# Optimization experiments

Hardware: AMD Instinct MI355X
Metric: run time of the kernel (lower is better)

Reference implementation:

```python
import jax, jax.numpy as jnp
import numpy as np

MASK_ID = -100
L, D, HID, NH = 10, 768, 3072, 12
DH = D // NH
REACH = 2  # (sliding_window_size - 1) // 2 with window 5


def _layernorm(x, g, b, eps=1e-5):
    mu = x.mean(-1, keepdims=True)
    var = ((x - mu) ** 2).mean(-1, keepdims=True)
    return (x - mu) * jax.lax.rsqrt(var + eps) * g + b


def _adaln(x, temb, w, bb, g, be):
    # AdaLayerNormShiftScale: linear(silu(temb)) -> (scale, shift)
    e = jax.nn.silu(temb) @ w + bb
    scale, shift = jnp.split(e, 2, axis=-1)
    return _layernorm(x, g, be) * (1.0 + scale) + shift


def _timestep_emb(t):
    half = D // 2
    exponent = -np.log(10000.0) * jnp.arange(half, dtype=jnp.float32) / (half - 1.0)
    freq = jnp.exp(exponent)  # [half]
    emb = t.astype(jnp.float32)[..., None] * freq  # [b,s,half]
    return jnp.concatenate([jnp.sin(emb), jnp.cos(emb)], axis=-1)  # [b,s,D]


def setup_inputs():
    key = jax.random.key(0)
    ks = jax.random.split(key, 16)
    b, s = 4, 1024
    # packed token ids: 4 samples of 256 tokens (16x16 grid), last 64 tokens padding
    idx = np.arange(s)
    sid = idx // 256
    hpos = (idx % 256) // 16
    wpos = idx % 16
    sid = np.where(idx >= 960, MASK_ID, sid)
    tok = np.stack([sid, hpos, wpos], axis=-1)  # [s,3]
    token_ids = jnp.asarray(np.broadcast_to(tok, (b, s, 3)).copy(), dtype=jnp.int32)
    t = jax.random.randint(ks[0], (b, 1), 0, L + 1).astype(jnp.int32)
    t = jnp.broadcast_to(t, (b, s))

    def w(k, shape):
        return jax.random.normal(k, shape, jnp.float32) * 0.02

    return dict(
        x=jax.random.normal(ks[1], (b, s, D), jnp.float32),
        t=t,
        token_ids=token_ids,
        proj_in_w=w(ks[2], (D, D)), proj_in_b=jnp.zeros((D,), jnp.float32),
        h_emb=w(ks[3], (64, D)), w_emb=w(ks[4], (64, D)),
        adaln1_w=w(ks[5], (L, D, 2 * D)), adaln1_b=jnp.zeros((L, 2 * D), jnp.float32),
        ln1_g=jnp.ones((L, D), jnp.float32), ln1_b=jnp.zeros((L, D), jnp.float32),
        qkv_w=w(ks[6], (L, D, 3 * D)), qkv_b=jnp.zeros((L, 3 * D), jnp.float32),
        o_w=w(ks[7], (L, D, D)), o_b=jnp.zeros((L, D), jnp.float32),
        adaln2_w=w(ks[8], (L, D, 2 * D)), adaln2_b=jnp.zeros((L, 2 * D), jnp.float32),
        ln2_g=jnp.ones((L, D), jnp.float32), ln2_b=jnp.zeros((L, D), jnp.float32),
        fc1_w=w(ks[9], (L, D, HID)), fc1_b=jnp.zeros((L, HID), jnp.float32),
        fc2_w=w(ks[10], (L, HID, D)), fc2_b=jnp.zeros((L, D), jnp.float32),
        nout_w=w(ks[11], (D, 2 * D)), nout_b=jnp.zeros((2 * D,), jnp.float32),
        nout_g=jnp.ones((D,), jnp.float32), nout_beta=jnp.zeros((D,), jnp.float32),
    )


def _encoder(x, t, token_ids, proj_in_w, proj_in_b, h_emb, w_emb,
             adaln1_w, adaln1_b, ln1_g, ln1_b, qkv_w, qkv_b, o_w, o_b,
             adaln2_w, adaln2_b, ln2_g, ln2_b, fc1_w, fc1_b, fc2_w, fc2_b,
             nout_w, nout_b, nout_g, nout_beta):
    b, s, _ = x.shape
    sample_ids = token_ids[..., 0]          # [b,s]
    pos = token_ids[..., 1:]                # [b,s,2]
    x = x @ proj_in_w + proj_in_b
    x = x + h_emb[pos[..., 0]] + w_emb[pos[..., 1]]

    # block-sparse mask: same packed sample, Chebyshev sliding window, no padding queries
    same = sample_ids[:, :, None] == sample_ids[:, None, :]              # [b,s,s]
    cheby = jnp.abs(pos[:, :, None, :] - pos[:, None, :, :]).max(-1)      # [b,s,s]
    notpad_q = (sample_ids != MASK_ID)[:, :, None]
    mask = same & (cheby <= REACH) & notpad_q                             # [b,s,s]
    row_valid = mask.any(-1)[..., None]                                   # [b,s,1]

    temb = _timestep_emb(t)  # [b,s,D]
    scale = 1.0 / np.sqrt(DH)
    for i in range(L):
        h1 = _adaln(x, temb, adaln1_w[i], adaln1_b[i], ln1_g[i], ln1_b[i])
        qkv = h1 @ qkv_w[i] + qkv_b[i]
        q, k, v = jnp.split(qkv, 3, axis=-1)
        q = q.reshape(b, s, NH, DH)
        k = k.reshape(b, s, NH, DH)
        v = v.reshape(b, s, NH, DH)
        scores = jnp.einsum('bqhd,bkhd->bhqk', q, k) * scale
        scores = jnp.where(mask[:, None], scores, -1e30)
        attn = jax.nn.softmax(scores, axis=-1)
        o = jnp.einsum('bhqk,bkhd->bqhd', attn, v).reshape(b, s, D)
        o = jnp.where(row_valid, o, 0.0)  # fully-masked (padding) rows -> 0
        x = x + o @ o_w[i] + o_b[i]
        h2 = _adaln(x, temb, adaln2_w[i], adaln2_b[i], ln2_g[i], ln2_b[i])
        x = x + jax.nn.gelu(h2 @ fc1_w[i] + fc1_b[i], approximate=False) @ fc2_w[i] + fc2_b[i]
    x = _adaln(x, temb, nout_w, nout_b, nout_g, nout_beta)
    return x


def reference(x, t, token_ids, proj_in_w, proj_in_b, h_emb, w_emb,
              adaln1_w, adaln1_b, ln1_g, ln1_b, qkv_w, qkv_b, o_w, o_b,
              adaln2_w, adaln2_b, ln2_g, ln2_b, fc1_w, fc1_b, fc2_w, fc2_b,
              nout_w, nout_b, nout_g, nout_beta):
    return _encoder(x, t, token_ids, proj_in_w, proj_in_b, h_emb, w_emb,
                    adaln1_w, adaln1_b, ln1_g, ln1_b, qkv_w, qkv_b, o_w, o_b,
                    adaln2_w, adaln2_b, ln2_g, ln2_b, fc1_w, fc1_b, fc2_w, fc2_b,
                    nout_w, nout_b, nout_g, nout_beta)
```

## Files before the change

### kernel.cpp

```cpp
#include <hip/hip_runtime.h>
#include <hip/hip_bf16.h>
#include <math.h>

#define MASK_ID (-100)
#define SEQ 1024
#define BATCH 4
#define DMODEL 768
#define NHEAD 12
#define DHEAD 64
#define NLAYER 10
#define HIDDEN 3072

typedef unsigned short ushort_t;
typedef unsigned int uint_t;

__device__ __forceinline__ ushort_t f2bf(float f) {
    uint_t u = __float_as_uint(f);
    u = u + 0x7fffu + ((u >> 16) & 1u);
    return (ushort_t)(u >> 16);
}
__device__ __forceinline__ float bf2f(ushort_t u) {
    return __uint_as_float(((uint_t)u) << 16);
}

__device__ __forceinline__ void async_ld16(ushort_t* lds, const ushort_t* g) {
    __builtin_amdgcn_global_load_lds((__attribute__((address_space(1))) const void*)g,
                                     (__attribute__((address_space(3))) void*)lds, 16, 0, 0);
}

#define WAITVM(n) asm volatile("s_waitcnt vmcnt(" #n ")" ::: "memory")

__global__ void temb_silu_kernel(const int* __restrict__ t, float* __restrict__ stemb) {
    int b = blockIdx.x;
    int j = threadIdx.x;
    float tv = (float)t[b * SEQ];
    float freq = expf(-logf(10000.f) * (float)j / 383.f);
    float arg = tv * freq;
    float s = sinf(arg), c = cosf(arg);
    stemb[b * DMODEL + j]       = s / (1.f + expf(-s));
    stemb[b * DMODEL + 384 + j] = c / (1.f + expf(-c));
}

__global__ __launch_bounds__(256)
void adaln_partial_kernel(const float* __restrict__ stemb,
                          const float* __restrict__ a1w,
                          const float* __restrict__ a2w,
                          const float* __restrict__ nw,
                          float* __restrict__ partial) {
    int chunk = blockIdx.x;
    int kc    = blockIdx.y;
    int slot  = blockIdx.z;
    int tid = threadIdx.x;
    int col = chunk * 256 + tid;
    const float* W;
    if (slot == 20) W = nw;
    else {
        int i = slot >> 1;
        W = ((slot & 1) ? a2w : a1w) + (size_t)i * DMODEL * 2 * DMODEL;
    }
    __shared__ float sb[4 * 96];
    for (int idx = tid; idx < 4 * 96; idx += 256) {
        int bb = idx / 96, kk = idx % 96;
        sb[idx] = stemb[bb * DMODEL + kc * 96 + kk];
    }
    __syncthreads();
    const float* Wp = W + (size_t)(kc * 96) * (2 * DMODEL) + col;
    float a0 = 0.f, a1 = 0.f, a2 = 0.f, a3 = 0.f;
    #pragma unroll 4
    for (int kk = 0; kk < 96; ++kk) {
        float w = Wp[(size_t)kk * (2 * DMODEL)];
        a0 = fmaf(sb[kk], w, a0);
        a1 = fmaf(sb[96 + kk], w, a1);
        a2 = fmaf(sb[192 + kk], w, a2);
        a3 = fmaf(sb[288 + kk], w, a3);
    }
    size_t base = ((size_t)(slot * 8 + kc) * 4) * (2 * DMODEL) + col;
    partial[base + 0 * 2 * DMODEL] = a0;
    partial[base + 1 * 2 * DMODEL] = a1;
    partial[base + 2 * 2 * DMODEL] = a2;
    partial[base + 3 * 2 * DMODEL] = a3;
}

__global__ __launch_bounds__(256)
void adaln_reduce_kernel(const float* __restrict__ partial,
                         const float* __restrict__ a1b, const float* __restrict__ a2b,
                         const float* __restrict__ nb,
                         float* __restrict__ e_all) {
    int chunk = blockIdx.x;
    int slot  = blockIdx.y;
    int col = chunk * 256 + threadIdx.x;
    const float* bb;
    if (slot == 20) bb = nb;
    else {
        int i = slot >> 1;
        bb = ((slot & 1) ? a2b : a1b) + i * 2 * DMODEL;
    }
    float bias = bb[col];
    float s0 = bias, s1 = bias, s2 = bias, s3 = bias;
    #pragma unroll
    for (int kc = 0; kc < 8; ++kc) {
        size_t base = ((size_t)(slot * 8 + kc) * 4) * (2 * DMODEL) + col;
        s0 += partial[base + 0 * 2 * DMODEL];
        s1 += partial[base + 1 * 2 * DMODEL];
        s2 += partial[base + 2 * 2 * DMODEL];
        s3 += partial[base + 3 * 2 * DMODEL];
    }
    size_t o = (size_t)slot * 4 * (2 * DMODEL) + col;
    e_all[o + 0 * 2 * DMODEL] = s0;
    e_all[o + 1 * 2 * DMODEL] = s1;
    e_all[o + 2 * 2 * DMODEL] = s2;
    e_all[o + 3 * 2 * DMODEL] = s3;
}

__global__ __launch_bounds__(256)
void transpose_bf16_kernel(const float* __restrict__ in, ushort_t* __restrict__ out,
                           int R, int C) {
    __shared__ float tile[32][33];
    int tx = threadIdx.x & 31, ty = threadIdx.x >> 5;
    int c0 = blockIdx.x * 32, r0 = blockIdx.y * 32;
    #pragma unroll
    for (int i = 0; i < 4; ++i)
        tile[ty + 8 * i][tx] = in[(size_t)(r0 + ty + 8 * i) * C + c0 + tx];
    __syncthreads();
    #pragma unroll
    for (int i = 0; i < 4; ++i)
        out[(size_t)(c0 + ty + 8 * i) * R + r0 + tx] = f2bf(tile[tx][ty + 8 * i]);
}

__global__ __launch_bounds__(256)
void transpose_all_kernel(const float* __restrict__ w0, const float* __restrict__ w1,
                          const float* __restrict__ w2, const float* __restrict__ w3,
                          ushort_t* __restrict__ o0, ushort_t* __restrict__ o1,
                          ushort_t* __restrict__ o2, ushort_t* __restrict__ o3) {
    int layer = blockIdx.y;
    int id = blockIdx.x;
    const float* in; ushort_t* out; int R, C, tile_id, TX;
    if (id < 216) {
        in = w0 + (size_t)layer * DMODEL * 3 * DMODEL; out = o0 + (size_t)layer * 3 * DMODEL * DMODEL;
        R = DMODEL; C = 3 * DMODEL; tile_id = id; TX = 36;
    } else if (id < 288) {
        in = w1 + (size_t)layer * DMODEL * DMODEL; out = o1 + (size_t)layer * DMODEL * DMODEL;
        R = DMODEL; C = DMODEL; tile_id = id - 216; TX = 12;
    } else if (id < 576) {
        in = w2 + (size_t)layer * DMODEL * HIDDEN; out = o2 + (size_t)layer * HIDDEN * DMODEL;
        R = DMODEL; C = HIDDEN; tile_id = id - 288; TX = 48;
    } else {
        in = w3 + (size_t)layer * HIDDEN * DMODEL; out = o3 + (size_t)layer * DMODEL * HIDDEN;
        R = HIDDEN; C = DMODEL; tile_id = id - 576; TX = 12;
    }
    int c0 = (tile_id % TX) * 64, r0 = (tile_id / TX) * 128;
    __shared__ float tl[128][65];
    int tid = threadIdx.x;
    #pragma unroll
    for (int i = 0; i < 32; ++i) {
        int idx = i * 256 + tid;
        int r = idx >> 6, c = idx & 63;
        tl[r][c] = in[(size_t)(r0 + r) * C + c0 + c];
    }
    __syncthreads();
    #pragma unroll
    for (int j = 0; j < 16; ++j) {
        int idx = j * 256 + tid;
        int oc = idx >> 6, pr = idx & 63;
        float a = tl[pr * 2][oc], b = tl[pr * 2 + 1][oc];
        uint_t pk = (uint_t)f2bf(a) | ((uint_t)f2bf(b) << 16);
        *(uint_t*)&out[(size_t)(c0 + oc) * R + r0 + pr * 2] = pk;
    }
}

__global__ __launch_bounds__(256)
void f32_to_bf16_kernel(const float* __restrict__ in, ushort_t* __restrict__ out, int n8) {
    int i = blockIdx.x * 256 + threadIdx.x;
    if (i >= n8) return;
    float4 a = ((const float4*)in)[2 * i];
    float4 b = ((const float4*)in)[2 * i + 1];
    uint4 o;
    o.x = (uint_t)f2bf(a.x) | ((uint_t)f2bf(a.y) << 16);
    o.y = (uint_t)f2bf(a.z) | ((uint_t)f2bf(a.w) << 16);
    o.z = (uint_t)f2bf(b.x) | ((uint_t)f2bf(b.y) << 16);
    o.w = (uint_t)f2bf(b.z) | ((uint_t)f2bf(b.w) << 16);
    ((uint4*)out)[i] = o;
}

template<int OUT_BF>
__global__ __launch_bounds__(256)
void ln_adaln_kernel(const float* __restrict__ in, void* __restrict__ outv,
                     const float* __restrict__ g, const float* __restrict__ be,
                     const float* __restrict__ e) {
    int wid = threadIdx.x >> 6, lane = threadIdx.x & 63;
    int row = blockIdx.x * 4 + wid;
    int b = row >> 10;
    const float* xr = in + (size_t)row * DMODEL;
    float v[12];
    float s = 0.f, ss = 0.f;
    #pragma unroll
    for (int j = 0; j < 12; ++j) {
        v[j] = xr[lane + j * 64];
        s += v[j];
        ss = fmaf(v[j], v[j], ss);
    }
    #pragma unroll
    for (int o = 1; o < 64; o <<= 1) { s += __shfl_xor(s, o); ss += __shfl_xor(ss, o); }
    float mu = s * (1.f / DMODEL);
    float var = ss * (1.f / DMODEL) - mu * mu;
    float rs = rsqrtf(var + 1e-5f);
    const float* esc = e + (size_t)b * (2 * DMODEL);
    #pragma unroll
    for (int j = 0; j < 12; ++j) {
        int c = lane + j * 64;
        float y = (v[j] - mu) * rs * g[c] + be[c];
        y = y * (1.f + esc[c]) + esc[DMODEL + c];
        if (OUT_BF) ((ushort_t*)outv)[(size_t)row * DMODEL + c] = f2bf(y);
        else        ((float*)outv)[(size_t)row * DMODEL + c] = y;
    }
}

__device__ __forceinline__ float gelu_exact(float x) {
    return 0.5f * x * (1.f + erff(x * 0.70710678118654752f));
}

template<int BM, int BN, int EPI, int OCC>
__global__ __launch_bounds__(256, OCC)
void gemm_bf16(const ushort_t* __restrict__ A, const ushort_t* __restrict__ Wt,
               const float* __restrict__ bias, void* __restrict__ outv,
               const float* __restrict__ emb_h, const float* __restrict__ emb_w,
               const int* __restrict__ tok,
               int M, int N, int K) {
    constexpr int WM = BM / 2, WN = BN / 2;
    constexpr int FM = WM / 16, FN = WN / 16;
    constexpr int BUF = (BM + BN) * 64;
    constexpr int LPT = (BM + BN) / 32;
    using f32x4  = __attribute__((ext_vector_type(4))) float;
    using bf16x8 = __attribute__((ext_vector_type(8))) short;

    __shared__ __align__(16) ushort_t lds[3 * BUF];

    int tid = threadIdx.x;
    int lane = tid & 63, wid = tid >> 6;
    int wr = wid >> 1, wc = wid & 1;
    int l16 = lane & 15, lg = lane >> 4;
    int sw = l16 & 7;

    int nx = N / BN;
    int cpx = gridDim.x >> 3;
    int wg = blockIdx.x;
    int wgid = (wg & 7) * cpx + (wg >> 3);
    int bx = wgid % nx, by = wgid / nx;
    int bm0 = by * BM, bn0 = bx * BN;

    f32x4 acc[FM][FN];
    #pragma unroll
    for (int m = 0; m < FM; ++m)
        #pragma unroll
        for (int n = 0; n < FN; ++n)
            #pragma unroll
            for (int r = 0; r < 4; ++r) acc[m][n][r] = 0.f;

    const ushort_t* Abase = A + (size_t)bm0 * K;
    const ushort_t* Bbase = Wt + (size_t)bn0 * K;

    #define STAGE(bufi, kt)                                                             \
        do {                                                                            \
            _Pragma("unroll")                                                           \
            for (int s2 = 0; s2 < BM / 32; ++s2) {                                      \
                int ca = s2 * 256 + tid;                                                \
                int rw = ca >> 3, kcs = (ca & 7) ^ (rw & 7);                            \
                async_ld16(&lds[(bufi) * BUF + ca * 8],                                 \
                           Abase + (size_t)rw * K + (kt) * 64 + kcs * 8);               \
            }                                                                           \
            _Pragma("unroll")                                                           \
            for (int s2 = 0; s2 < BN / 32; ++s2) {                                      \
                int ca = s2 * 256 + tid;                                                \
                int rw = ca >> 3, kcs = (ca & 7) ^ (rw & 7);                            \
                async_ld16(&lds[(bufi) * BUF + BM * 64 + ca * 8],                       \
                           Bbase + (size_t)rw * K + (kt) * 64 + kcs * 8);               \
            }                                                                           \
        } while (0)

    int nk = K >> 6;
    STAGE(0, 0);
    STAGE(1, 1);
    int bufi = 0;
    for (int kt = 0; kt < nk; ++kt) {
        int nxt = bufi + 2; if (nxt >= 3) nxt -= 3;
        if (kt + 2 < nk) {
            STAGE(nxt, kt + 2);
            if constexpr (LPT == 4) WAITVM(8); else WAITVM(12);
        } else if (kt + 1 < nk) {
            if constexpr (LPT == 4) WAITVM(4); else WAITVM(6);
        } else {
            WAITVM(0);
        }
        __builtin_amdgcn_s_barrier();
        __builtin_amdgcn_s_setprio(1);
        #pragma unroll
        for (int kk = 0; kk < 2; ++kk) {
            bf16x8 af[FM], bfr[FN];
            #pragma unroll
            for (int m = 0; m < FM; ++m) {
                int row = wr * WM + m * 16 + l16;
                int csw = (kk * 4 + lg) ^ sw;
                af[m] = *(const bf16x8*)&lds[bufi * BUF + row * 64 + csw * 8];
            }
            #pragma unroll
            for (int n = 0; n < FN; ++n) {
                int row = wc * WN + n * 16 + l16;
                int csw = (kk * 4 + lg) ^ sw;
                bfr[n] = *(const bf16x8*)&lds[bufi * BUF + BM * 64 + row * 64 + csw * 8];
            }
            #pragma unroll
            for (int m = 0; m < FM; ++m)
                #pragma unroll
                for (int n = 0; n < FN; ++n)
                    acc[m][n] = __builtin_amdgcn_mfma_f32_16x16x32_bf16(af[m], bfr[n], acc[m][n], 0, 0, 0);
        }
        __builtin_amdgcn_s_setprio(0);
        __builtin_amdgcn_s_barrier();
        ++bufi; if (bufi >= 3) bufi = 0;
    }
    #undef STAGE

    int r0 = bm0 + wr * WM, c0 = bn0 + wc * WN;
    #pragma unroll
    for (int m = 0; m < FM; ++m) {
        #pragma unroll
        for (int n = 0; n < FN; ++n) {
            int cc = c0 + n * 16 + l16;
            float bcol = bias[cc];
            #pragma unroll
            for (int r = 0; r < 4; ++r) {
                int row = r0 + m * 16 + lg * 4 + r;
                float v = acc[m][n][r] + bcol;
                if (EPI == 0) {
                    ((ushort_t*)outv)[(size_t)row * N + cc] = f2bf(v);
                } else if (EPI == 1) {
                    int p0 = tok[row * 3 + 1], p1 = tok[row * 3 + 2];
                    v += emb_h[p0 * DMODEL + cc] + emb_w[p1 * DMODEL + cc];
                    ((float*)outv)[(size_t)row * N + cc] = v;
                } else if (EPI == 2) {
                    float* op = (float*)outv + (size_t)row * N + cc;
                    *op = *op + v;
                } else {
                    ((ushort_t*)outv)[(size_t)row * N + cc] = f2bf(gelu_exact(v));
                }
            }
        }
    }
}

__global__ __launch_bounds__(256)
void attn_kernel(const ushort_t* __restrict__ qkv, const int* __restrict__ tok,
                 ushort_t* __restrict__ o_out) {
    int tid = threadIdx.x;
    int u = tid >> 2, part = tid & 3;
    int q = blockIdx.x * 16 + (u & 15);
    int h = blockIdx.y * 4 + (u >> 4);
    int b = blockIdx.z;
    int m = b * SEQ + q;
    ushort_t* op = o_out + (size_t)m * DMODEL + h * DHEAD + part * 16;
    int sid = tok[m * 3];
    if (sid == MASK_ID) {
        uint4 z = {0u, 0u, 0u, 0u};
        ((uint4*)op)[0] = z;
        ((uint4*)op)[1] = z;
        return;
    }
    int qh = tok[m * 3 + 1], qw = tok[m * 3 + 2];
    const ushort_t* qp = qkv + (size_t)m * (3 * DMODEL) + h * DHEAD + part * 16;
    float qv[16], ov[16];
    {
        uint4 u0 = ((const uint4*)qp)[0];
        uint4 u1 = ((const uint4*)qp)[1];
        qv[0] = bf2f(u0.x & 0xffff); qv[1] = bf2f(u0.x >> 16);
        qv[2] = bf2f(u0.y & 0xffff); qv[3] = bf2f(u0.y >> 16);
        qv[4] = bf2f(u0.z & 0xffff); qv[5] = bf2f(u0.z >> 16);
        qv[6] = bf2f(u0.w & 0xffff); qv[7] = bf2f(u0.w >> 16);
        qv[8]  = bf2f(u1.x & 0xffff); qv[9]  = bf2f(u1.x >> 16);
        qv[10] = bf2f(u1.y & 0xffff); qv[11] = bf2f(u1.y >> 16);
        qv[12] = bf2f(u1.z & 0xffff); qv[13] = bf2f(u1.z >> 16);
        qv[14] = bf2f(u1.w & 0xffff); qv[15] = bf2f(u1.w >> 16);
    }
    #pragma unroll
    for (int i = 0; i < 16; ++i) ov[i] = 0.f;
    float mx = -1e30f, den = 0.f;
    for (int dh = -2; dh <= 2; ++dh) {
        for (int dw = -2; dw <= 2; ++dw) {
            int kq = q + dh * 16 + dw;
            if (kq < 0 || kq >= SEQ) continue;
            int km = b * SEQ + kq;
            if (tok[km * 3] != sid) continue;
            int kh2 = tok[km * 3 + 1], kw2 = tok[km * 3 + 2];
            int adh = kh2 - qh; if (adh < 0) adh = -adh;
            int adw = kw2 - qw; if (adw < 0) adw = -adw;
            if (adh > 2 || adw > 2) continue;
            const ushort_t* kp = qkv + (size_t)km * (3 * DMODEL) + DMODEL + h * DHEAD + part * 16;
            float dot;
            {
                uint4 u0 = ((const uint4*)kp)[0];
                uint4 u1 = ((const uint4*)kp)[1];
                dot = qv[0] * bf2f(u0.x & 0xffff);
                dot = fmaf(qv[1], bf2f(u0.x >> 16), dot);
                dot = fmaf(qv[2], bf2f(u0.y & 0xffff), dot);
                dot = fmaf(qv[3], bf2f(u0.y >> 16), dot);
                dot = fmaf(qv[4], bf2f(u0.z & 0xffff), dot);
                dot = fmaf(qv[5], bf2f(u0.z >> 16), dot);
                dot = fmaf(qv[6], bf2f(u0.w & 0xffff), dot);
                dot = fmaf(qv[7], bf2f(u0.w >> 16), dot);
                dot = fmaf(qv[8],  bf2f(u1.x & 0xffff), dot);
                dot = fmaf(qv[9],  bf2f(u1.x >> 16), dot);
                dot = fmaf(qv[10], bf2f(u1.y & 0xffff), dot);
                dot = fmaf(qv[11], bf2f(u1.y >> 16), dot);
                dot = fmaf(qv[12], bf2f(u1.z & 0xffff), dot);
                dot = fmaf(qv[13], bf2f(u1.z >> 16), dot);
                dot = fmaf(qv[14], bf2f(u1.w & 0xffff), dot);
                dot = fmaf(qv[15], bf2f(u1.w >> 16), dot);
            }
            dot += __shfl_xor(dot, 1);
            dot += __shfl_xor(dot, 2);
            float sc = dot * 0.125f;
            float nm = fmaxf(mx, sc);
            float c1 = expf(mx - nm);
            float c2 = expf(sc - nm);
            den = den * c1 + c2;
            const ushort_t* vp = qkv + (size_t)km * (3 * DMODEL) + 2 * DMODEL + h * DHEAD + part * 16;
            {
                uint4 u0 = ((const uint4*)vp)[0];
                uint4 u1 = ((const uint4*)vp)[1];
                ov[0] = ov[0] * c1 + c2 * bf2f(u0.x & 0xffff);
                ov[1] = ov[1] * c1 + c2 * bf2f(u0.x >> 16);
                ov[2] = ov[2] * c1 + c2 * bf2f(u0.y & 0xffff);
                ov[3] = ov[3] * c1 + c2 * bf2f(u0.y >> 16);
                ov[4] = ov[4] * c1 + c2 * bf2f(u0.z & 0xffff);
                ov[5] = ov[5] * c1 + c2 * bf2f(u0.z >> 16);
                ov[6] = ov[6] * c1 + c2 * bf2f(u0.w & 0xffff);
                ov[7] = ov[7] * c1 + c2 * bf2f(u0.w >> 16);
                ov[8]  = ov[8]  * c1 + c2 * bf2f(u1.x & 0xffff);
                ov[9]  = ov[9]  * c1 + c2 * bf2f(u1.x >> 16);
                ov[10] = ov[10] * c1 + c2 * bf2f(u1.y & 0xffff);
                ov[11] = ov[11] * c1 + c2 * bf2f(u1.y >> 16);
                ov[12] = ov[12] * c1 + c2 * bf2f(u1.z & 0xffff);
                ov[13] = ov[13] * c1 + c2 * bf2f(u1.z >> 16);
                ov[14] = ov[14] * c1 + c2 * bf2f(u1.w & 0xffff);
                ov[15] = ov[15] * c1 + c2 * bf2f(u1.w >> 16);
            }
            mx = nm;
        }
    }
    float inv = 1.f / den;
    uint4 o0, o1;
    o0.x = (uint_t)f2bf(ov[0] * inv) | ((uint_t)f2bf(ov[1] * inv) << 16);
    o0.y = (uint_t)f2bf(ov[2] * inv) | ((uint_t)f2bf(ov[3] * inv) << 16);
    o0.z = (uint_t)f2bf(ov[4] * inv) | ((uint_t)f2bf(ov[5] * inv) << 16);
    o0.w = (uint_t)f2bf(ov[6] * inv) | ((uint_t)f2bf(ov[7] * inv) << 16);
    o1.x = (uint_t)f2bf(ov[8]  * inv) | ((uint_t)f2bf(ov[9]  * inv) << 16);
    o1.y = (uint_t)f2bf(ov[10] * inv) | ((uint_t)f2bf(ov[11] * inv) << 16);
    o1.z = (uint_t)f2bf(ov[12] * inv) | ((uint_t)f2bf(ov[13] * inv) << 16);
    o1.w = (uint_t)f2bf(ov[14] * inv) | ((uint_t)f2bf(ov[15] * inv) << 16);
    ((uint4*)op)[0] = o0;
    ((uint4*)op)[1] = o1;
}

extern "C" void kernel_launch(void* const* d_in, const int* in_sizes, int n_in,
                              void* d_out, int out_size, void* d_ws, size_t ws_size,
                              hipStream_t stream) {
    const float* x_in      = (const float*)d_in[0];
    const int*   t         = (const int*)d_in[1];
    const int*   tok       = (const int*)d_in[2];
    const float* proj_in_w = (const float*)d_in[3];
    const float* proj_in_b = (const float*)d_in[4];
    const float* h_emb     = (const float*)d_in[5];
    const float* w_emb     = (const float*)d_in[6];
    const float* adaln1_w  = (const float*)d_in[7];
    const float* adaln1_b  = (const float*)d_in[8];
    const float* ln1_g     = (const float*)d_in[9];
    const float* ln1_b     = (const float*)d_in[10];
    const float* qkv_w     = (const float*)d_in[11];
    const float* qkv_b     = (const float*)d_in[12];
    const float* o_w       = (const float*)d_in[13];
    const float* o_b       = (const float*)d_in[14];
    const float* adaln2_w  = (const float*)d_in[15];
    const float* adaln2_b  = (const float*)d_in[16];
    const float* ln2_g     = (const float*)d_in[17];
    const float* ln2_b     = (const float*)d_in[18];
    const float* fc1_w     = (const float*)d_in[19];
    const float* fc1_b     = (const float*)d_in[20];
    const float* fc2_w     = (const float*)d_in[21];
    const float* fc2_b     = (const float*)d_in[22];
    const float* nout_w    = (const float*)d_in[23];
    const float* nout_b    = (const float*)d_in[24];
    const float* nout_g    = (const float*)d_in[25];
    const float* nout_beta = (const float*)d_in[26];

    const int M = BATCH * SEQ;

    float* stemb   = (float*)d_ws;
    float* e_all   = stemb + BATCH * DMODEL;
    float* partial = e_all + 21 * BATCH * 2 * DMODEL;
    ushort_t* h_bf   = (ushort_t*)(partial + 21 * 8 * 4 * 2 * DMODEL);
    ushort_t* qkv_bf = h_bf + (size_t)M * DMODEL;
    ushort_t* hid_bf = qkv_bf + (size_t)M * 3 * DMODEL;
    ushort_t* projT  = hid_bf + (size_t)M * HIDDEN;
    ushort_t* qkvT_a = projT + (size_t)DMODEL * DMODEL;
    ushort_t* oT_a   = qkvT_a + (size_t)NLAYER * 3 * DMODEL * DMODEL;
    ushort_t* fc1T_a = oT_a + (size_t)NLAYER * DMODEL * DMODEL;
    ushort_t* fc2T_a = fc1T_a + (size_t)NLAYER * DMODEL * HIDDEN;
    float* x = (float*)d_out;

    temb_silu_kernel<<<BATCH, 384, 0, stream>>>(t, stemb);
    adaln_partial_kernel<<<dim3(6, 8, 2 * NLAYER + 1), 256, 0, stream>>>(
        stemb, adaln1_w, adaln2_w, nout_w, partial);
    adaln_reduce_kernel<<<dim3(6, 2 * NLAYER + 1), 256, 0, stream>>>(
        partial, adaln1_b, adaln2_b, nout_b, e_all);

    transpose_all_kernel<<<dim3(864, NLAYER), 256, 0, stream>>>(
        qkv_w, o_w, fc1_w, fc2_w, qkvT_a, oT_a, fc1T_a, fc2T_a);
    transpose_bf16_kernel<<<dim3(DMODEL / 32, DMODEL / 32), 256, 0, stream>>>(proj_in_w, projT, DMODEL, DMODEL);

    f32_to_bf16_kernel<<<(M * DMODEL / 8 + 255) / 256, 256, 0, stream>>>(x_in, h_bf, M * DMODEL / 8);
    gemm_bf16<64, 64, 1, 3><<<(DMODEL / 64) * (M / 64), 256, 0, stream>>>(
        h_bf, projT, proj_in_b, x, h_emb, w_emb, tok, M, DMODEL, DMODEL);

    for (int i = 0; i < NLAYER; ++i) {
        ln_adaln_kernel<1><<<M / 4, 256, 0, stream>>>(
            x, h_bf, ln1_g + i * DMODEL, ln1_b + i * DMODEL,
            e_all + (size_t)(2 * i) * BATCH * 2 * DMODEL);
        gemm_bf16<64, 128, 0, 2><<<(3 * DMODEL / 128) * (M / 64), 256, 0, stream>>>(
            h_bf, qkvT_a + (size_t)i * 3 * DMODEL * DMODEL, qkv_b + i * 3 * DMODEL,
            qkv_bf, nullptr, nullptr, nullptr, M, 3 * DMODEL, DMODEL);
        attn_kernel<<<dim3(SEQ / 16, NHEAD / 4, BATCH), 256, 0, stream>>>(qkv_bf, tok, h_bf);
        gemm_bf16<64, 64, 2, 3><<<(DMODEL / 64) * (M / 64), 256, 0, stream>>>(
            h_bf, oT_a + (size_t)i * DMODEL * DMODEL, o_b + i * DMODEL,
            x, nullptr, nullptr, nullptr, M, DMODEL, DMODEL);
        ln_adaln_kernel<1><<<M / 4, 256, 0, stream>>>(
            x, h_bf, ln2_g + i * DMODEL, ln2_b + i * DMODEL,
            e_all + (size_t)(2 * i + 1) * BATCH * 2 * DMODEL);
        gemm_bf16<64, 128, 3, 2><<<(HIDDEN / 128) * (M / 64), 256, 0, stream>>>(
            h_bf, fc1T_a + (size_t)i * DMODEL * HIDDEN, fc1_b + i * HIDDEN,
            hid_bf, nullptr, nullptr, nullptr, M, HIDDEN, DMODEL);
        gemm_bf16<64, 64, 2, 3><<<(DMODEL / 64) * (M / 64), 256, 0, stream>>>(
            hid_bf, fc2T_a + (size_t)i * DMODEL * HIDDEN, fc2_b + i * DMODEL,
            x, nullptr, nullptr, nullptr, M, DMODEL, HIDDEN);
    }

    ln_adaln_kernel<0><<<M / 4, 256, 0, stream>>>(
        x, x, nout_g, nout_beta, e_all + (size_t)(2 * NLAYER) * BATCH * 2 * DMODEL);
}
```

Before: 1.839 ms.

## Use 128x128 single-buffer GEMM for QKV/FC1 and shrink transpose tiles

Adds a new gemm_bf16_big kernel with 128x128 block tiles, 4x4 MFMA fragments per wave, XCD-aware block remapping and a single LDS buffer, and uses it for the QKV and FC1 projections. The larger tile raises arithmetic intensity per loaded byte, but the single buffer gives up the triple-buffered load/compute overlap of the old kernel. The weight transpose kernel also switches to 64x64 tiles staged in LDS as bf16, halving shared memory and doubling the grid.

```diff
diff --git a/kernel.cpp b/kernel.cpp
--- a/kernel.cpp
+++ b/kernel.cpp
@@ -135,35 +135,34 @@
     int layer = blockIdx.y;
     int id = blockIdx.x;
     const float* in; ushort_t* out; int R, C, tile_id, TX;
-    if (id < 216) {
+    if (id < 432) {
         in = w0 + (size_t)layer * DMODEL * 3 * DMODEL; out = o0 + (size_t)layer * 3 * DMODEL * DMODEL;
         R = DMODEL; C = 3 * DMODEL; tile_id = id; TX = 36;
-    } else if (id < 288) {
+    } else if (id < 576) {
         in = w1 + (size_t)layer * DMODEL * DMODEL; out = o1 + (size_t)layer * DMODEL * DMODEL;
-        R = DMODEL; C = DMODEL; tile_id = id - 216; TX = 12;
-    } else if (id < 576) {
+        R = DMODEL; C = DMODEL; tile_id = id - 432; TX = 12;
+    } else if (id < 1152) {
         in = w2 + (size_t)layer * DMODEL * HIDDEN; out = o2 + (size_t)layer * HIDDEN * DMODEL;
-        R = DMODEL; C = HIDDEN; tile_id = id - 288; TX = 48;
+        R = DMODEL; C = HIDDEN; tile_id = id - 576; TX = 48;
     } else {
         in = w3 + (size_t)layer * HIDDEN * DMODEL; out = o3 + (size_t)layer * DMODEL * HIDDEN;
-        R = HIDDEN; C = DMODEL; tile_id = id - 576; TX = 12;
-    }
-    int c0 = (tile_id % TX) * 64, r0 = (tile_id / TX) * 128;
-    __shared__ float tl[128][65];
+        R = HIDDEN; C = DMODEL; tile_id = id - 1152; TX = 12;
+    }
+    int c0 = (tile_id % TX) * 64, r0 = (tile_id / TX) * 64;
+    __shared__ ushort_t tlb[64 * 65];
     int tid = threadIdx.x;
     #pragma unroll
-    for (int i = 0; i < 32; ++i) {
+    for (int i = 0; i < 16; ++i) {
         int idx = i * 256 + tid;
         int r = idx >> 6, c = idx & 63;
-        tl[r][c] = in[(size_t)(r0 + r) * C + c0 + c];
+        tlb[r * 65 + c] = f2bf(in[(size_t)(r0 + r) * C + c0 + c]);
     }
     __syncthreads();
     #pragma unroll
-    for (int j = 0; j < 16; ++j) {
+    for (int j = 0; j < 8; ++j) {
         int idx = j * 256 + tid;
-        int oc = idx >> 6, pr = idx & 63;
-        float a = tl[pr * 2][oc], b = tl[pr * 2 + 1][oc];
-        uint_t pk = (uint_t)f2bf(a) | ((uint_t)f2bf(b) << 16);
+        int oc = idx >> 5, pr = idx & 31;
+        uint_t pk = (uint_t)tlb[(pr * 2) * 65 + oc] | ((uint_t)tlb[(pr * 2 + 1) * 65 + oc] << 16);
         *(uint_t*)&out[(size_t)(c0 + oc) * R + r0 + pr * 2] = pk;
     }
 }
@@ -217,6 +216,94 @@
 
 __device__ __forceinline__ float gelu_exact(float x) {
     return 0.5f * x * (1.f + erff(x * 0.70710678118654752f));
+}
+
+template<int EPI>
+__global__ __launch_bounds__(256, 3)
+void gemm_bf16_big(const ushort_t* __restrict__ A, const ushort_t* __restrict__ Wt,
+                   const float* __restrict__ bias, void* __restrict__ outv,
+                   int M, int N, int K) {
+    constexpr int BM = 128, BN = 128;
+    using f32x4  = __attribute__((ext_vector_type(4))) float;
+    using bf16x8 = __attribute__((ext_vector_type(8))) short;
+
+    __shared__ __align__(16) ushort_t lds[(BM + BN) * 64];
+
+    int tid = threadIdx.x;
+    int lane = tid & 63, wid = tid >> 6;
+    int wr = wid >> 1, wc = wid & 1;
+    int l16 = lane & 15, lg = lane >> 4;
+    int sw = l16 & 7;
+
+    int nx = N / BN;
+    int cpx = gridDim.x >> 3;
+    int wg = blockIdx.x;
+    int wgid = (wg & 7) * cpx + (wg >> 3);
+    int bx = wgid % nx, by = wgid / nx;
+    int bm0 = by * BM, bn0 = bx * BN;
+
+    f32x4 acc[4][4];
+    #pragma unroll
+    for (int m = 0; m < 4; ++m)
+        #pragma unroll
+        for (int n = 0; n < 4; ++n)
+            #pragma unroll
+            for (int r = 0; r < 4; ++r) acc[m][n][r] = 0.f;
+
+    const ushort_t* Abase = A + (size_t)bm0 * K;
+    const ushort_t* Bbase = Wt + (size_t)bn0 * K;
+
+    int nk = K >> 6;
+    for (int kt = 0; kt < nk; ++kt) {
+        #pragma unroll
+        for (int s2 = 0; s2 < 4; ++s2) {
+            int ca = s2 * 256 + tid;
+            int rw = ca >> 3, kcs = (ca & 7) ^ (rw & 7);
+            async_ld16(&lds[ca * 8], Abase + (size_t)rw * K + kt * 64 + kcs * 8);
+        }
+        #pragma unroll
+        for (int s2 = 0; s2 < 4; ++s2) {
+            int ca = s2 * 256 + tid;
+            int rw = ca >> 3, kcs = (ca & 7) ^ (rw & 7);
+            async_ld16(&lds[BM * 64 + ca * 8], Bbase + (size_t)rw * K + kt * 64 + kcs * 8);
+        }
+        WAITVM(0);
+        __syncthreads();
+        #pragma unroll
+        for (int kk = 0; kk < 2; ++kk) {
+            int csw = (kk * 4 + lg) ^ sw;
+            bf16x8 af[4], bfr[4];
+            #pragma unroll
+            for (int m = 0; m < 4; ++m)
+                af[m] = *(const bf16x8*)&lds[(wr * 64 + m * 16 + l16) * 64 + csw * 8];
+            #pragma unroll
+            for (int n = 0; n < 4; ++n)
+                bfr[n] = *(const bf16x8*)&lds[BM * 64 + (wc * 64 + n * 16 + l16) * 64 + csw * 8];
+            #pragma unroll
+            for (int m = 0; m < 4; ++m)
+                #pragma unroll
+                for (int n = 0; n < 4; ++n)
+                    acc[m][n] = __builtin_amdgcn_mfma_f32_16x16x32_bf16(af[m], bfr[n], acc[m][n], 0, 0, 0);
+        }
+        __syncthreads();
+    }
+
+    int r0 = bm0 + wr * 64, c0 = bn0 + wc * 64;
+    #pragma unroll
+    for (int m = 0; m < 4; ++m) {
+        #pragma unroll
+        for (int n = 0; n < 4; ++n) {
+            int cc = c0 + n * 16 + l16;
+            float bcol = bias[cc];
+            #pragma unroll
+            for (int r = 0; r < 4; ++r) {
+                int row = r0 + m * 16 + lg * 4 + r;
+                float v = acc[m][n][r] + bcol;
+                if (EPI == 0) ((ushort_t*)outv)[(size_t)row * N + cc] = f2bf(v);
+                else          ((ushort_t*)outv)[(size_t)row * N + cc] = f2bf(gelu_exact(v));
+            }
+        }
+    }
 }
 
 template<int BM, int BN, int EPI, int OCC>
@@ -512,7 +599,7 @@
     adaln_reduce_kernel<<<dim3(6, 2 * NLAYER + 1), 256, 0, stream>>>(
         partial, adaln1_b, adaln2_b, nout_b, e_all);
 
-    transpose_all_kernel<<<dim3(864, NLAYER), 256, 0, stream>>>(
+    transpose_all_kernel<<<dim3(1728, NLAYER), 256, 0, stream>>>(
         qkv_w, o_w, fc1_w, fc2_w, qkvT_a, oT_a, fc1T_a, fc2T_a);
     transpose_bf16_kernel<<<dim3(DMODEL / 32, DMODEL / 32), 256, 0, stream>>>(proj_in_w, projT, DMODEL, DMODEL);
 
@@ -524,9 +611,9 @@
         ln_adaln_kernel<1><<<M / 4, 256, 0, stream>>>(
             x, h_bf, ln1_g + i * DMODEL, ln1_b + i * DMODEL,
             e_all + (size_t)(2 * i) * BATCH * 2 * DMODEL);
-        gemm_bf16<64, 128, 0, 2><<<(3 * DMODEL / 128) * (M / 64), 256, 0, stream>>>(
+        gemm_bf16_big<0><<<(3 * DMODEL / 128) * (M / 128), 256, 0, stream>>>(
             h_bf, qkvT_a + (size_t)i * 3 * DMODEL * DMODEL, qkv_b + i * 3 * DMODEL,
-            qkv_bf, nullptr, nullptr, nullptr, M, 3 * DMODEL, DMODEL);
+            qkv_bf, M, 3 * DMODEL, DMODEL);
         attn_kernel<<<dim3(SEQ / 16, NHEAD / 4, BATCH), 256, 0, stream>>>(qkv_bf, tok, h_bf);
         gemm_bf16<64, 64, 2, 3><<<(DMODEL / 64) * (M / 64), 256, 0, stream>>>(
             h_bf, oT_a + (size_t)i * DMODEL * DMODEL, o_b + i * DMODEL,
@@ -534,9 +621,9 @@
         ln_adaln_kernel<1><<<M / 4, 256, 0, stream>>>(
             x, h_bf, ln2_g + i * DMODEL, ln2_b + i * DMODEL,
             e_all + (size_t)(2 * i + 1) * BATCH * 2 * DMODEL);
-        gemm_bf16<64, 128, 3, 2><<<(HIDDEN / 128) * (M / 64), 256, 0, stream>>>(
+        gemm_bf16_big<3><<<(HIDDEN / 128) * (M / 128), 256, 0, stream>>>(
             h_bf, fc1T_a + (size_t)i * DMODEL * HIDDEN, fc1_b + i * HIDDEN,
-            hid_bf, nullptr, nullptr, nullptr, M, HIDDEN, DMODEL);
+            hid_bf, M, HIDDEN, DMODEL);
         gemm_bf16<64, 64, 2, 3><<<(DMODEL / 64) * (M / 64), 256, 0, stream>>>(
             hid_bf, fc2T_a + (size_t)i * DMODEL * HIDDEN, fc2_b + i * DMODEL,
             x, nullptr, nullptr, nullptr, M, DMODEL, HIDDEN);
```

After: 1.685 ms. 1.09x faster.
